# Kernel tuning notes

Hardware: AMD Instinct MI355X
Metric: run time of the kernel (lower is better)

## Reference

```python
import jax, jax.numpy as jnp
import numpy as np

H = 31   # hidden_size
IN = 36  # input_size
NC = 7   # num_classes
B = 1024
T = 512


def setup_inputs() -> dict:
    key = jax.random.key(0)
    ks = jax.random.split(key, 19)
    s = 1.0 / np.sqrt(H)  # PyTorch GRU init range
    u = lambda k, shape: jax.random.uniform(k, shape, jnp.float32, -s, s)
    inp = {"x": jax.random.normal(ks[0], (B, T, IN), jnp.float32)}
    i = 1
    for l, din in ((0, IN), (1, 2 * H)):
        for d in ("f", "b"):
            inp[f"W_ih_l{l}{d}"] = u(ks[i], (3 * H, din)); i += 1
            inp[f"W_hh_l{l}{d}"] = u(ks[i], (3 * H, H)); i += 1
            inp[f"b_ih_l{l}{d}"] = u(ks[i], (3 * H,)); i += 1
            inp[f"b_hh_l{l}{d}"] = u(ks[i], (3 * H,)); i += 1
    inp["fc_w"] = u(ks[17], (NC, 2 * H))
    inp["fc_b"] = u(ks[18], (NC,))
    return inp


def _gru_dir(x, Wih, Whh, bih, bhh, reverse):
    # x: [B,T,F]; precompute input-side gates for all timesteps in one GEMM
    xg = jnp.einsum('btf,gf->btg', x, Wih) + bih  # [B,T,3H]
    if reverse:
        xg = xg[:, ::-1]

    def step(h, xt):
        hg = h @ Whh.T + bhh                      # [B,3H]
        xr, xz, xn = jnp.split(xt, 3, axis=-1)    # PyTorch gate order: r,z,n
        hr, hz, hn = jnp.split(hg, 3, axis=-1)
        r = jax.nn.sigmoid(xr + hr)
        z = jax.nn.sigmoid(xz + hz)
        n = jnp.tanh(xn + r * hn)
        h_new = (1.0 - z) * n + z * h
        return h_new, h_new

    h0 = jnp.zeros((x.shape[0], Whh.shape[1]), x.dtype)
    _, ys = jax.lax.scan(step, h0, jnp.swapaxes(xg, 0, 1))  # [T,B,H]
    ys = jnp.swapaxes(ys, 0, 1)                              # [B,T,H]
    return ys[:, ::-1] if reverse else ys


def _forward(x, params, fc_w, fc_b):
    h = x
    for pf, pb in params:  # 2 layers (structural loop)
        yf = _gru_dir(h, *pf, reverse=False)
        yb = _gru_dir(h, *pb, reverse=True)
        h = jnp.concatenate([yf, yb], axis=-1)  # [B,T,2H]
    last = h[:, -1, :]                          # out[:, -1, :]
    return last @ fc_w.T + fc_b                 # [B,NC]


def reference(x, W_ih_l0f, W_hh_l0f, b_ih_l0f, b_hh_l0f,
              W_ih_l0b, W_hh_l0b, b_ih_l0b, b_hh_l0b,
              W_ih_l1f, W_hh_l1f, b_ih_l1f, b_hh_l1f,
              W_ih_l1b, W_hh_l1b, b_ih_l1b, b_hh_l1b,
              fc_w, fc_b):
    params = [((W_ih_l0f, W_hh_l0f, b_ih_l0f, b_hh_l0f),
               (W_ih_l0b, W_hh_l0b, b_ih_l0b, b_hh_l0b)),
              ((W_ih_l1f, W_hh_l1f, b_ih_l1f, b_hh_l1f),
               (W_ih_l1b, W_hh_l1b, b_ih_l1b, b_hh_l1b))]
    return _forward(x, params, fc_w, fc_b)
```

## Files before the change

kernel.cpp:

```cpp
#include <hip/hip_runtime.h>
#include <hip/hip_bf16.h>


#define NB 1024
#define NT 512
#define NH 31
#define NG 93
#define NC 7

__device__ __forceinline__ float sig_(float x) { return 1.f / (1.f + __expf(-x)); }
__device__ __forceinline__ float th_(float x)  { float e = __expf(2.f * x); return (e - 1.f) / (e + 1.f); }

__device__ __forceinline__ float tf_(float v) { return v; }
__device__ __forceinline__ float tf_(__hip_bfloat16 v) { return __bfloat162float(v); }

__device__ __forceinline__ void ldpair(const float* p, float& a, float& b) {
    float2 v = *(const float2*)p; a = v.x; b = v.y;
}
__device__ __forceinline__ void ldpair(const __hip_bfloat16* p, float& a, float& b) {
    ushort2 u = *(const ushort2*)p;
    a = __uint_as_float((unsigned)u.x << 16);
    b = __uint_as_float((unsigned)u.y << 16);
}
__device__ __forceinline__ void stoy(float* p, float v) { *p = v; }
__device__ __forceinline__ void stoy(__hip_bfloat16* p, float v) { *p = __float2bfloat16(v); }

#define LOADX(arr, ptr)                                                   \
    _Pragma("unroll") for (int k_ = 0; k_ < KH; k_ += 2)                  \
        ldpair((ptr) + k_, arr[k_], arr[k_ + 1])

#define GRU_STEP(XV)                                                      \
    do {                                                                  \
        const float4 g0 = *(const float4*)&hbuf[w][hlo + 0];              \
        const float4 g1 = *(const float4*)&hbuf[w][hlo + 4];              \
        const float4 g2 = *(const float4*)&hbuf[w][hlo + 8];              \
        const float4 g3 = *(const float4*)&hbuf[w][hlo + 12];             \
        float hv[16];                                                     \
        hv[0]=g0.x;  hv[1]=g0.y;  hv[2]=g0.z;  hv[3]=g0.w;                \
        hv[4]=g1.x;  hv[5]=g1.y;  hv[6]=g1.z;  hv[7]=g1.w;                \
        hv[8]=g2.x;  hv[9]=g2.y;  hv[10]=g2.z; hv[11]=g2.w;               \
        hv[12]=g3.x; hv[13]=g3.y; hv[14]=g3.z; hv[15]=g3.w;               \
        float ar = b_r, az = b_z, an = b_xn, ah = b_hn;                   \
        _Pragma("unroll") for (int k_ = 0; k_ < KH; ++k_) {               \
            ar = fmaf(Wxr[k_], XV[k_], ar);                               \
            az = fmaf(Wxz[k_], XV[k_], az);                               \
            an = fmaf(Wxn[k_], XV[k_], an);                               \
        }                                                                 \
        _Pragma("unroll") for (int k_ = 0; k_ < 16; ++k_) {               \
            ar = fmaf(Whr[k_], hv[k_], ar);                               \
            az = fmaf(Whz[k_], hv[k_], az);                               \
            ah = fmaf(Whn[k_], hv[k_], ah);                               \
        }                                                                 \
        ar += __shfl_xor(ar, 32, 64);                                     \
        az += __shfl_xor(az, 32, 64);                                     \
        an += __shfl_xor(an, 32, 64);                                     \
        ah += __shfl_xor(ah, 32, 64);                                     \
        const float r_ = sig_(ar);                                        \
        const float z_ = sig_(az);                                        \
        const float n_ = th_(an + r_ * ah);                               \
        h_prev = n_ + z_ * (h_prev - n_);                                 \
        if (half == 0 && j < NH) {                                        \
            hbuf[w][j] = h_prev;                                          \
            if (WRITE_Y) stoy(yp, h_prev);                                \
        }                                                                 \
    } while (0)

template<typename XT, typename YT, int DIN, int KH, bool WRITE_Y, bool WRITE_HF>
__device__ __forceinline__ void gru_scan_body(
    const XT* __restrict__ xin,
    const float* __restrict__ Wih, const float* __restrict__ Whh,
    const float* __restrict__ bih, const float* __restrict__ bhh,
    int dir, YT* __restrict__ y, float* __restrict__ hf)
{
    static_assert((KH & 1) == 0, "even KH");
    const int tid  = threadIdx.x;
    const int w    = tid >> 6;
    const int lane = tid & 63;
    const int half = lane >> 5;
    const int j    = lane & 31;
    const int jj   = j < NH ? j : NH - 1;
    const int b    = blockIdx.x * 4 + w;

    __shared__ __align__(16) float hbuf[4][32];
    if (lane < 32) hbuf[w][lane] = 0.f;
    __syncthreads();

    const int klo = half ? (DIN - KH) : 0;

    float Wxr[KH], Wxz[KH], Wxn[KH];
#pragma unroll
    for (int k = 0; k < KH; ++k) {
        const bool v = half ? true : (k < DIN - KH);
        Wxr[k] = v ? Wih[(0 * NH + jj) * DIN + klo + k] : 0.f;
        Wxz[k] = v ? Wih[(1 * NH + jj) * DIN + klo + k] : 0.f;
        Wxn[k] = v ? Wih[(2 * NH + jj) * DIN + klo + k] : 0.f;
    }
    const int hlo = half * 16;
    float Whr[16], Whz[16], Whn[16];
#pragma unroll
    for (int k = 0; k < 16; ++k) {
        const bool v = (hlo + k) < NH;
        Whr[k] = v ? Whh[(0 * NH + jj) * NH + hlo + k] : 0.f;
        Whz[k] = v ? Whh[(1 * NH + jj) * NH + hlo + k] : 0.f;
        Whn[k] = v ? Whh[(2 * NH + jj) * NH + hlo + k] : 0.f;
    }
    float b_r = 0.f, b_z = 0.f, b_xn = 0.f, b_hn = 0.f;
    if (half == 0) {
        b_r  = bih[jj] + bhh[jj];
        b_z  = bih[NH + jj] + bhh[NH + jj];
        b_xn = bih[2 * NH + jj];
        b_hn = bhh[2 * NH + jj];
    }

    const XT* xrow = xin + (size_t)b * NT * DIN + klo
                   + (dir ? (size_t)(NT - 1) * DIN : 0);
    const ptrdiff_t xstep = dir ? -DIN : DIN;
    YT* yp = nullptr;
    ptrdiff_t ystep = 0;
    if (WRITE_Y) {
        yp = y + (size_t)b * NT * 62 + dir * NH + j
           + (dir ? (size_t)(NT - 1) * 62 : 0);
        ystep = dir ? -62 : 62;
    }

    float h_prev = 0.f;
    float xa[KH], xb[KH];
    LOADX(xa, xrow);
    const XT* xpre = xrow + xstep;

    for (int s = 0; s < NT; s += 2) {
        LOADX(xb, xpre);
        if (s + 2 < NT) xpre += xstep;
        GRU_STEP(xa);
        if (WRITE_Y) yp += ystep;
        LOADX(xa, xpre);
        if (s + 3 < NT) xpre += xstep;
        GRU_STEP(xb);
        if (WRITE_Y) yp += ystep;
    }
    if (WRITE_HF && half == 0 && j < NH) hf[b * NH + j] = h_prev;
}

template<typename YT>
__global__ void __launch_bounds__(256)
__attribute__((amdgpu_waves_per_eu(2, 2)))
gru_scan_l0(
    const float* __restrict__ x,
    const float* __restrict__ Wf, const float* __restrict__ Uf,
    const float* __restrict__ bf, const float* __restrict__ cf,
    const float* __restrict__ Wb, const float* __restrict__ Ub,
    const float* __restrict__ bb, const float* __restrict__ cb,
    YT* __restrict__ y)
{
    const int d = blockIdx.y;
    gru_scan_body<float, YT, 36, 18, true, false>(
        x, d ? Wb : Wf, d ? Ub : Uf, d ? bb : bf, d ? cb : cf, d, y, nullptr);
}

template<typename YT>
__global__ void __launch_bounds__(256)
__attribute__((amdgpu_waves_per_eu(1, 1)))
gru_scan_l1(
    const YT* __restrict__ y0,
    const float* __restrict__ W, const float* __restrict__ U,
    const float* __restrict__ bi, const float* __restrict__ bh,
    float* __restrict__ hf)
{
    gru_scan_body<YT, YT, 62, 32, false, true>(y0, W, U, bi, bh, 0, (YT*)nullptr, hf);
}

template<typename YT>
__global__ void __launch_bounds__(64, 4) gru_final(
    const YT* __restrict__ y0, const float* __restrict__ hf,
    const float* __restrict__ Wih1b, const float* __restrict__ bih1b,
    const float* __restrict__ bhh1b,
    const float* __restrict__ fcw, const float* __restrict__ fcb,
    float* __restrict__ out)
{
    const int b = blockIdx.x;
    const int lane = threadIdx.x;
    __shared__ float row[62];
    __shared__ float xg[NG];
    __shared__ float last[62];
    const YT* yl = y0 + ((size_t)b * NT + (NT - 1)) * 62;
    if (lane < 62) row[lane] = tf_(yl[lane]);
    __syncthreads();
    for (int g = lane; g < NG; g += 64) {
        float a = bih1b[g];
        const float* wr = Wih1b + g * 62;
#pragma unroll
        for (int k = 0; k < 62; ++k) a = fmaf(wr[k], row[k], a);
        xg[g] = a;
    }
    if (lane < NH) last[lane] = hf[b * NH + lane];
    __syncthreads();
    if (lane < NH) {
        const float r = sig_(xg[lane] + bhh1b[lane]);
        const float z = sig_(xg[NH + lane] + bhh1b[NH + lane]);
        const float n = th_(xg[2 * NH + lane] + r * bhh1b[2 * NH + lane]);
        last[NH + lane] = (1.f - z) * n;
    }
    __syncthreads();
    if (lane < NC) {
        float a = fcb[lane];
        const float* wr = fcw + lane * 62;
#pragma unroll
        for (int k = 0; k < 62; ++k) a = fmaf(wr[k], last[k], a);
        out[b * NC + lane] = a;
    }
}

extern "C" void kernel_launch(void* const* d_in, const int* in_sizes, int n_in,
                              void* d_out, int out_size, void* d_ws, size_t ws_size,
                              hipStream_t stream)
{
    const float* x     = (const float*)d_in[0];
    const float* Wih0f = (const float*)d_in[1];
    const float* Whh0f = (const float*)d_in[2];
    const float* bih0f = (const float*)d_in[3];
    const float* bhh0f = (const float*)d_in[4];
    const float* Wih0b = (const float*)d_in[5];
    const float* Whh0b = (const float*)d_in[6];
    const float* bih0b = (const float*)d_in[7];
    const float* bhh0b = (const float*)d_in[8];
    const float* Wih1f = (const float*)d_in[9];
    const float* Whh1f = (const float*)d_in[10];
    const float* bih1f = (const float*)d_in[11];
    const float* bhh1f = (const float*)d_in[12];
    const float* Wih1b = (const float*)d_in[13];
    const float* Whh1b = (const float*)d_in[14];
    const float* bih1b = (const float*)d_in[15];
    const float* bhh1b = (const float*)d_in[16];
    const float* fcw   = (const float*)d_in[17];
    const float* fcb   = (const float*)d_in[18];
    float* out = (float*)d_out;
    (void)Whh1b; (void)in_sizes; (void)n_in; (void)out_size;

    const size_t y0_elems  = (size_t)NB * NT * 62;
    const size_t hf_bytes  = (size_t)NB * NH * 4;
    const size_t need_f32  = y0_elems * 4 + 256 + hf_bytes;
    const size_t need_bf16 = y0_elems * 2 + 256 + hf_bytes;

    const dim3 blk(256);
    if (ws_size >= need_f32) {
        float* y0 = (float*)d_ws;
        float* hf = (float*)((char*)d_ws + ((y0_elems * 4 + 255) & ~(size_t)255));
        gru_scan_l0<float><<<dim3(NB / 4, 2), blk, 0, stream>>>(
            x, Wih0f, Whh0f, bih0f, bhh0f, Wih0b, Whh0b, bih0b, bhh0b, y0);
        gru_scan_l1<float><<<dim3(NB / 4, 1), blk, 0, stream>>>(
            y0, Wih1f, Whh1f, bih1f, bhh1f, hf);
        gru_final<float><<<dim3(NB), dim3(64), 0, stream>>>(
            y0, hf, Wih1b, bih1b, bhh1b, fcw, fcb, out);
    } else if (ws_size >= need_bf16) {
        __hip_bfloat16* y0 = (__hip_bfloat16*)d_ws;
        float* hf = (float*)((char*)d_ws + ((y0_elems * 2 + 255) & ~(size_t)255));
        gru_scan_l0<__hip_bfloat16><<<dim3(NB / 4, 2), blk, 0, stream>>>(
            x, Wih0f, Whh0f, bih0f, bhh0f, Wih0b, Whh0b, bih0b, bhh0b, y0);
        gru_scan_l1<__hip_bfloat16><<<dim3(NB / 4, 1), blk, 0, stream>>>(
            y0, Wih1f, Whh1f, bih1f, bhh1f, hf);
        gru_final<__hip_bfloat16><<<dim3(NB), dim3(64), 0, stream>>>(
            y0, hf, Wih1b, bih1b, bhh1b, fcw, fcb, out);
    }
}
```

Before: 556.8 us.

## Move GRU weights from registers to LDS and drop bf16 fallback path

The per-lane weight arrays (input and recurrent gate weights) move out of VGPRs into a padded shared-memory table. Each step now reads them with float4 LDS loads instead of holding them in registers. This is meant to cut register pressure, but it adds LDS traffic to every timestep of the serial recurrence. The bf16 workspace fallback is removed, so the fp32 intermediate is always used regardless of workspace size.

```diff
diff --git a/kernel.cpp b/kernel.cpp
--- a/kernel.cpp
+++ b/kernel.cpp
@@ -1,5 +1,4 @@
 #include <hip/hip_runtime.h>
-#include <hip/hip_bf16.h>
 
 
 #define NB 1024
@@ -7,29 +6,12 @@
 #define NH 31
 #define NG 93
 #define NC 7
+#define BT (NB * NT)
 
 __device__ __forceinline__ float sig_(float x) { return 1.f / (1.f + __expf(-x)); }
 __device__ __forceinline__ float th_(float x)  { float e = __expf(2.f * x); return (e - 1.f) / (e + 1.f); }
 
-__device__ __forceinline__ float tf_(float v) { return v; }
-__device__ __forceinline__ float tf_(__hip_bfloat16 v) { return __bfloat162float(v); }
-
-__device__ __forceinline__ void ldpair(const float* p, float& a, float& b) {
-    float2 v = *(const float2*)p; a = v.x; b = v.y;
-}
-__device__ __forceinline__ void ldpair(const __hip_bfloat16* p, float& a, float& b) {
-    ushort2 u = *(const ushort2*)p;
-    a = __uint_as_float((unsigned)u.x << 16);
-    b = __uint_as_float((unsigned)u.y << 16);
-}
-__device__ __forceinline__ void stoy(float* p, float v) { *p = v; }
-__device__ __forceinline__ void stoy(__hip_bfloat16* p, float v) { *p = __float2bfloat16(v); }
-
-#define LOADX(arr, ptr)                                                   \
-    _Pragma("unroll") for (int k_ = 0; k_ < KH; k_ += 2)                  \
-        ldpair((ptr) + k_, arr[k_], arr[k_ + 1])
-
-#define GRU_STEP(XV)                                                      \
+#define STEPB(XV)                                                         \
     do {                                                                  \
         const float4 g0 = *(const float4*)&hbuf[w][hlo + 0];              \
         const float4 g1 = *(const float4*)&hbuf[w][hlo + 4];              \
@@ -41,15 +23,39 @@
         hv[8]=g2.x;  hv[9]=g2.y;  hv[10]=g2.z; hv[11]=g2.w;               \
         hv[12]=g3.x; hv[13]=g3.y; hv[14]=g3.z; hv[15]=g3.w;               \
         float ar = b_r, az = b_z, an = b_xn, ah = b_hn;                   \
-        _Pragma("unroll") for (int k_ = 0; k_ < KH; ++k_) {               \
-            ar = fmaf(Wxr[k_], XV[k_], ar);                               \
-            az = fmaf(Wxz[k_], XV[k_], az);                               \
-            an = fmaf(Wxn[k_], XV[k_], an);                               \
+        _Pragma("unroll") for (int q = 0; q < WXP / 4; ++q) {             \
+            const float4 wr = *(const float4*)(wl + 0 * WXP + q * 4);     \
+            const float4 wz = *(const float4*)(wl + 1 * WXP + q * 4);     \
+            const float4 wn = *(const float4*)(wl + 2 * WXP + q * 4);     \
+            ar = fmaf(wr.x, XV[q*4+0], ar);                               \
+            ar = fmaf(wr.y, XV[q*4+1], ar);                               \
+            ar = fmaf(wr.z, XV[q*4+2], ar);                               \
+            ar = fmaf(wr.w, XV[q*4+3], ar);                               \
+            az = fmaf(wz.x, XV[q*4+0], az);                               \
+            az = fmaf(wz.y, XV[q*4+1], az);                               \
+            az = fmaf(wz.z, XV[q*4+2], az);                               \
+            az = fmaf(wz.w, XV[q*4+3], az);                               \
+            an = fmaf(wn.x, XV[q*4+0], an);                               \
+            an = fmaf(wn.y, XV[q*4+1], an);                               \
+            an = fmaf(wn.z, XV[q*4+2], an);                               \
+            an = fmaf(wn.w, XV[q*4+3], an);                               \
         }                                                                 \
-        _Pragma("unroll") for (int k_ = 0; k_ < 16; ++k_) {               \
-            ar = fmaf(Whr[k_], hv[k_], ar);                               \
-            az = fmaf(Whz[k_], hv[k_], az);                               \
-            ah = fmaf(Whn[k_], hv[k_], ah);                               \
+        _Pragma("unroll") for (int q = 0; q < 4; ++q) {                   \
+            const float4 ur = *(const float4*)(wl + 3 * WXP +      q * 4);\
+            const float4 uz = *(const float4*)(wl + 3 * WXP + 16 + q * 4);\
+            const float4 un = *(const float4*)(wl + 3 * WXP + 32 + q * 4);\
+            ar = fmaf(ur.x, hv[q*4+0], ar);                               \
+            ar = fmaf(ur.y, hv[q*4+1], ar);                               \
+            ar = fmaf(ur.z, hv[q*4+2], ar);                               \
+            ar = fmaf(ur.w, hv[q*4+3], ar);                               \
+            az = fmaf(uz.x, hv[q*4+0], az);                               \
+            az = fmaf(uz.y, hv[q*4+1], az);                               \
+            az = fmaf(uz.z, hv[q*4+2], az);                               \
+            az = fmaf(uz.w, hv[q*4+3], az);                               \
+            ah = fmaf(un.x, hv[q*4+0], ah);                               \
+            ah = fmaf(un.y, hv[q*4+1], ah);                               \
+            ah = fmaf(un.z, hv[q*4+2], ah);                               \
+            ah = fmaf(un.w, hv[q*4+3], ah);                               \
         }                                                                 \
         ar += __shfl_xor(ar, 32, 64);                                     \
         az += __shfl_xor(az, 32, 64);                                     \
@@ -61,18 +67,19 @@
         h_prev = n_ + z_ * (h_prev - n_);                                 \
         if (half == 0 && j < NH) {                                        \
             hbuf[w][j] = h_prev;                                          \
-            if (WRITE_Y) stoy(yp, h_prev);                                \
+            if (WRITE_Y) *yp = h_prev;                                    \
         }                                                                 \
+        if (WRITE_Y) yp += ystep;                                         \
     } while (0)
 
-template<typename XT, typename YT, int DIN, int KH, bool WRITE_Y, bool WRITE_HF>
-__device__ __forceinline__ void gru_scan_body(
-    const XT* __restrict__ xin,
+template<int DIN, int KH, int WXP, int WSTR, bool WRITE_Y, bool WRITE_HF>
+__device__ __forceinline__ void lds_scan(
+    const float* __restrict__ xin,
     const float* __restrict__ Wih, const float* __restrict__ Whh,
     const float* __restrict__ bih, const float* __restrict__ bhh,
-    int dir, YT* __restrict__ y, float* __restrict__ hf)
-{
-    static_assert((KH & 1) == 0, "even KH");
+    int dir, float* __restrict__ y, float* __restrict__ hf)
+{
+    static_assert((KH & 1) == 0 && (WXP & 3) == 0 && (WSTR & 7) == 4, "layout");
     const int tid  = threadIdx.x;
     const int w    = tid >> 6;
     const int lane = tid & 63;
@@ -82,28 +89,24 @@
     const int b    = blockIdx.x * 4 + w;
 
     __shared__ __align__(16) float hbuf[4][32];
+    __shared__ __align__(16) float wlds[64][WSTR];
+
+    const int klo = half ? (DIN - KH) : 0;
+    const int hlo = half * 16;
+
+    if (w < 3) {
+        const int g = w;
+        for (int k = 0; k < WXP; ++k) {
+            const bool v = (k < KH) && (half ? true : (k < DIN - KH));
+            wlds[lane][g * WXP + k] = v ? Wih[(g * NH + jj) * DIN + klo + k] : 0.f;
+        }
+        for (int k = 0; k < 16; ++k) {
+            const bool v = (hlo + k) < NH;
+            wlds[lane][3 * WXP + g * 16 + k] = v ? Whh[(g * NH + jj) * NH + hlo + k] : 0.f;
+        }
+    }
     if (lane < 32) hbuf[w][lane] = 0.f;
-    __syncthreads();
-
-    const int klo = half ? (DIN - KH) : 0;
-
-    float Wxr[KH], Wxz[KH], Wxn[KH];
-#pragma unroll
-    for (int k = 0; k < KH; ++k) {
-        const bool v = half ? true : (k < DIN - KH);
-        Wxr[k] = v ? Wih[(0 * NH + jj) * DIN + klo + k] : 0.f;
-        Wxz[k] = v ? Wih[(1 * NH + jj) * DIN + klo + k] : 0.f;
-        Wxn[k] = v ? Wih[(2 * NH + jj) * DIN + klo + k] : 0.f;
-    }
-    const int hlo = half * 16;
-    float Whr[16], Whz[16], Whn[16];
-#pragma unroll
-    for (int k = 0; k < 16; ++k) {
-        const bool v = (hlo + k) < NH;
-        Whr[k] = v ? Whh[(0 * NH + jj) * NH + hlo + k] : 0.f;
-        Whz[k] = v ? Whh[(1 * NH + jj) * NH + hlo + k] : 0.f;
-        Whn[k] = v ? Whh[(2 * NH + jj) * NH + hlo + k] : 0.f;
-    }
+
     float b_r = 0.f, b_z = 0.f, b_xn = 0.f, b_hn = 0.f;
     if (half == 0) {
         b_r  = bih[jj] + bhh[jj];
@@ -111,11 +114,14 @@
         b_xn = bih[2 * NH + jj];
         b_hn = bhh[2 * NH + jj];
     }
-
-    const XT* xrow = xin + (size_t)b * NT * DIN + klo
-                   + (dir ? (size_t)(NT - 1) * DIN : 0);
+    __syncthreads();
+
+    const float* wl = &wlds[lane][0];
+
+    const float* xrow = xin + (size_t)b * NT * DIN + klo
+                      + (dir ? (size_t)(NT - 1) * DIN : 0);
     const ptrdiff_t xstep = dir ? -DIN : DIN;
-    YT* yp = nullptr;
+    float* yp = nullptr;
     ptrdiff_t ystep = 0;
     if (WRITE_Y) {
         yp = y + (size_t)b * NT * 62 + dir * NH + j
@@ -124,54 +130,58 @@
     }
 
     float h_prev = 0.f;
-    float xa[KH], xb[KH];
-    LOADX(xa, xrow);
-    const XT* xpre = xrow + xstep;
+    float xa[WXP], xb[WXP];
+#pragma unroll
+    for (int k = 0; k < WXP; ++k) { xa[k] = 0.f; xb[k] = 0.f; }
+#pragma unroll
+    for (int k = 0; k < KH; k += 2) {
+        float2 v = *(const float2*)(xrow + k); xa[k] = v.x; xa[k + 1] = v.y;
+    }
+    const float* xpre = xrow + xstep;
 
     for (int s = 0; s < NT; s += 2) {
-        LOADX(xb, xpre);
+#pragma unroll
+        for (int k = 0; k < KH; k += 2) {
+            float2 v = *(const float2*)(xpre + k); xb[k] = v.x; xb[k + 1] = v.y;
+        }
         if (s + 2 < NT) xpre += xstep;
-        GRU_STEP(xa);
-        if (WRITE_Y) yp += ystep;
-        LOADX(xa, xpre);
+        STEPB(xa);
+#pragma unroll
+        for (int k = 0; k < KH; k += 2) {
+            float2 v = *(const float2*)(xpre + k); xa[k] = v.x; xa[k + 1] = v.y;
+        }
         if (s + 3 < NT) xpre += xstep;
-        GRU_STEP(xb);
-        if (WRITE_Y) yp += ystep;
-    }
-    if (WRITE_HF && half == 0 && j < NH) hf[b * NH + j] = h_prev;
-}
-
-template<typename YT>
+        STEPB(xb);
+    }
+    if (WRITE_HF && half == 0 && j < NH) hf[(size_t)b * NH + j] = h_prev;
+}
+
 __global__ void __launch_bounds__(256)
 __attribute__((amdgpu_waves_per_eu(2, 2)))
-gru_scan_l0(
-    const float* __restrict__ x,
-    const float* __restrict__ Wf, const float* __restrict__ Uf,
-    const float* __restrict__ bf, const float* __restrict__ cf,
-    const float* __restrict__ Wb, const float* __restrict__ Ub,
-    const float* __restrict__ bb, const float* __restrict__ cb,
-    YT* __restrict__ y)
+gru_scan_l0(const float* __restrict__ x,
+            const float* __restrict__ Wf, const float* __restrict__ Uf,
+            const float* __restrict__ bf, const float* __restrict__ cf,
+            const float* __restrict__ Wb, const float* __restrict__ Ub,
+            const float* __restrict__ bb, const float* __restrict__ cb,
+            float* __restrict__ y)
 {
     const int d = blockIdx.y;
-    gru_scan_body<float, YT, 36, 18, true, false>(
+    lds_scan<36, 18, 20, 108, true, false>(
         x, d ? Wb : Wf, d ? Ub : Uf, d ? bb : bf, d ? cb : cf, d, y, nullptr);
 }
 
-template<typename YT>
 __global__ void __launch_bounds__(256)
 __attribute__((amdgpu_waves_per_eu(1, 1)))
-gru_scan_l1(
-    const YT* __restrict__ y0,
-    const float* __restrict__ W, const float* __restrict__ U,
-    const float* __restrict__ bi, const float* __restrict__ bh,
-    float* __restrict__ hf)
-{
-    gru_scan_body<YT, YT, 62, 32, false, true>(y0, W, U, bi, bh, 0, (YT*)nullptr, hf);
-}
-
-template<typename YT>
+gru_scan_l1(const float* __restrict__ y0,
+            const float* __restrict__ W, const float* __restrict__ U,
+            const float* __restrict__ bi, const float* __restrict__ bh,
+            float* __restrict__ hf)
+{
+    lds_scan<62, 32, 32, 148, false, true>(y0, W, U, bi, bh, 0, nullptr, hf);
+}
+
 __global__ void __launch_bounds__(64, 4) gru_final(
-    const YT* __restrict__ y0, const float* __restrict__ hf,
+    const float* __restrict__ y0, const float* __restrict__ hf,
     const float* __restrict__ Wih1b, const float* __restrict__ bih1b,
     const float* __restrict__ bhh1b,
     const float* __restrict__ fcw, const float* __restrict__ fcb,
@@ -180,24 +190,24 @@
     const int b = blockIdx.x;
     const int lane = threadIdx.x;
     __shared__ float row[62];
-    __shared__ float xg[NG];
+    __shared__ float xgs[NG];
     __shared__ float last[62];
-    const YT* yl = y0 + ((size_t)b * NT + (NT - 1)) * 62;
-    if (lane < 62) row[lane] = tf_(yl[lane]);
+    const float* yl = y0 + ((size_t)b * NT + (NT - 1)) * 62;
+    if (lane < 62) row[lane] = yl[lane];
     __syncthreads();
     for (int g = lane; g < NG; g += 64) {
         float a = bih1b[g];
         const float* wr = Wih1b + g * 62;
 #pragma unroll
         for (int k = 0; k < 62; ++k) a = fmaf(wr[k], row[k], a);
-        xg[g] = a;
-    }
-    if (lane < NH) last[lane] = hf[b * NH + lane];
+        xgs[g] = a;
+    }
+    if (lane < NH) last[lane] = hf[(size_t)b * NH + lane];
     __syncthreads();
     if (lane < NH) {
-        const float r = sig_(xg[lane] + bhh1b[lane]);
-        const float z = sig_(xg[NH + lane] + bhh1b[NH + lane]);
-        const float n = th_(xg[2 * NH + lane] + r * bhh1b[2 * NH + lane]);
+        const float r = sig_(xgs[lane] + bhh1b[lane]);
+        const float z = sig_(xgs[NH + lane] + bhh1b[NH + lane]);
+        const float n = th_(xgs[2 * NH + lane] + r * bhh1b[2 * NH + lane]);
         last[NH + lane] = (1.f - z) * n;
     }
     __syncthreads();
@@ -209,6 +219,7 @@
         out[b * NC + lane] = a;
     }
 }
+
 
 extern "C" void kernel_launch(void* const* d_in, const int* in_sizes, int n_in,
                               void* d_out, int out_size, void* d_ws, size_t ws_size,
@@ -234,31 +245,17 @@
     const float* fcw   = (const float*)d_in[17];
     const float* fcb   = (const float*)d_in[18];
     float* out = (float*)d_out;
-    (void)Whh1b; (void)in_sizes; (void)n_in; (void)out_size;
-
-    const size_t y0_elems  = (size_t)NB * NT * 62;
-    const size_t hf_bytes  = (size_t)NB * NH * 4;
-    const size_t need_f32  = y0_elems * 4 + 256 + hf_bytes;
-    const size_t need_bf16 = y0_elems * 2 + 256 + hf_bytes;
+    (void)Whh1b; (void)in_sizes; (void)n_in; (void)out_size; (void)ws_size;
+
+    const size_t y0_elems = (size_t)BT * 62;
+    float* y0 = (float*)d_ws;
+    float* hf = (float*)((char*)d_ws + ((y0_elems * 4 + 255) & ~(size_t)255));
 
     const dim3 blk(256);
-    if (ws_size >= need_f32) {
-        float* y0 = (float*)d_ws;
-        float* hf = (float*)((char*)d_ws + ((y0_elems * 4 + 255) & ~(size_t)255));
-        gru_scan_l0<float><<<dim3(NB / 4, 2), blk, 0, stream>>>(
-            x, Wih0f, Whh0f, bih0f, bhh0f, Wih0b, Whh0b, bih0b, bhh0b, y0);
-        gru_scan_l1<float><<<dim3(NB / 4, 1), blk, 0, stream>>>(
-            y0, Wih1f, Whh1f, bih1f, bhh1f, hf);
-        gru_final<float><<<dim3(NB), dim3(64), 0, stream>>>(
-            y0, hf, Wih1b, bih1b, bhh1b, fcw, fcb, out);
-    } else if (ws_size >= need_bf16) {
-        __hip_bfloat16* y0 = (__hip_bfloat16*)d_ws;
-        float* hf = (float*)((char*)d_ws + ((y0_elems * 2 + 255) & ~(size_t)255));
-        gru_scan_l0<__hip_bfloat16><<<dim3(NB / 4, 2), blk, 0, stream>>>(
-            x, Wih0f, Whh0f, bih0f, bhh0f, Wih0b, Whh0b, bih0b, bhh0b, y0);
-        gru_scan_l1<__hip_bfloat16><<<dim3(NB / 4, 1), blk, 0, stream>>>(
-            y0, Wih1f, Whh1f, bih1f, bhh1f, hf);
-        gru_final<__hip_bfloat16><<<dim3(NB), dim3(64), 0, stream>>>(
-            y0, hf, Wih1b, bih1b, bhh1b, fcw, fcb, out);
-    }
-}
+    gru_scan_l0<<<dim3(NB / 4, 2), blk, 0, stream>>>(
+        x, Wih0f, Whh0f, bih0f, bhh0f, Wih0b, Whh0b, bih0b, bhh0b, y0);
+    gru_scan_l1<<<dim3(NB / 4, 1), blk, 0, stream>>>(
+        y0, Wih1f, Whh1f, bih1f, bhh1f, hf);
+    gru_final<<<dim3(NB), dim3(64), 0, stream>>>(
+        y0, hf, Wih1b, bih1b, bhh1b, fcw, fcb, out);
+}
```

Result: no change. 563.6 us (+1.2%).
